# Kernel optimization log

Hardware: AMD Instinct MI355X
Metric: run time of the kernel (lower is better)

Reference implementation:

```python
import jax, jax.numpy as jnp
import numpy as np

T = 16                       # sample_duration
FG_THRESH, BG_HI, BG_LO = 0.5, 0.5, 0.1
ROIS_PER_IMAGE, FG_PER_IMAGE = 128, 32   # conf.TRAIN.BATCH_SIZE, round(0.25*128)
STDS = jnp.tile(jnp.array([0.1, 0.1, 0.2, 0.2], jnp.float32), T)  # BBOX_NORMALIZE_STDS tiled; means are 0


def _tube_iou(rois, gts):
    # rois [b,M,T,4], gts [b,K,T,4] -> mean per-frame IoU over non-empty frames [b,M,K]
    r = rois[:, :, None]             # [b,M,1,T,4]
    g = gts[:, None]                 # [b,1,K,T,4]
    iw = jnp.clip(jnp.minimum(r[..., 2], g[..., 2]) - jnp.maximum(r[..., 0], g[..., 0]) + 1.0, 0.0)
    ih = jnp.clip(jnp.minimum(r[..., 3], g[..., 3]) - jnp.maximum(r[..., 1], g[..., 1]) + 1.0, 0.0)
    inter = iw * ih
    ar = (r[..., 2] - r[..., 0] + 1.0) * (r[..., 3] - r[..., 1] + 1.0)
    ag = (g[..., 2] - g[..., 0] + 1.0) * (g[..., 3] - g[..., 1] + 1.0)
    r_empty = jnp.all(r == 0.0, -1)
    g_empty = jnp.all(g == 0.0, -1)
    iou = jnp.where(r_empty | g_empty, 0.0, inter / (ar + ag - inter))
    valid = ~(r_empty & g_empty)
    return iou.sum(-1) / jnp.maximum(valid.sum(-1), 1).astype(iou.dtype)


def _bbox_transform(ex, gt):
    ew = ex[..., 2] - ex[..., 0] + 1.0
    eh = ex[..., 3] - ex[..., 1] + 1.0
    ecx = ex[..., 0] + 0.5 * ew
    ecy = ex[..., 1] + 0.5 * eh
    gw = gt[..., 2] - gt[..., 0] + 1.0
    gh = gt[..., 3] - gt[..., 1] + 1.0
    gcx = gt[..., 0] + 0.5 * gw
    gcy = gt[..., 1] + 0.5 * gh
    return jnp.stack([(gcx - ecx) / ew, (gcy - ecy) / eh,
                      jnp.log(gw / ew), jnp.log(gh / eh)], axis=-1)


def _sample_one(ov, lab, key):
    # ov, lab: [M]; jit-safe fg/bg sampling matching the torch control flow
    M = ov.shape[0]
    k1, k2, k3, k4 = jax.random.split(key, 4)
    fg = ov >= FG_THRESH
    bg = (ov < BG_HI) & (ov >= BG_LO)
    fg_num = fg.sum()
    bg_num = bg.sum()
    # random permutation with fg (resp. bg) indices first
    order_fg = jnp.argsort(jnp.where(fg, jax.random.uniform(k1, (M,)), 2.0))
    order_bg = jnp.argsort(jnp.where(bg, jax.random.uniform(k2, (M,)), 2.0))
    fg_this = jnp.where(bg_num > 0, jnp.minimum(FG_PER_IMAGE, fg_num),
                        jnp.where(fg_num > 0, ROIS_PER_IMAGE, 0))
    r = jnp.arange(ROIS_PER_IMAGE)
    fg_repl = order_fg[(jax.random.uniform(k3, (ROIS_PER_IMAGE,)) * jnp.maximum(fg_num, 1)).astype(jnp.int32)]
    fg_idx = jnp.where(bg_num > 0, order_fg[r], fg_repl)  # no-replacement when bg exists, else with replacement
    bg_idx = order_bg[(jax.random.uniform(k4, (ROIS_PER_IMAGE,)) * jnp.maximum(bg_num, 1)).astype(jnp.int32)]
    is_fg = r < fg_this
    keep = jnp.where(is_fg, fg_idx, bg_idx)
    return keep, jnp.where(is_fg, lab[keep], 0.0)


def _forward(all_tubes, gt_boxes, gt_tubes_all):
    b, N, _ = all_tubes.shape
    A = gt_boxes.shape[1]
    # gt tube coords + label of first nonzero-labelled frame
    gt_tubes = gt_boxes[..., :4].reshape(b, A, T * 4)
    fr_lab = gt_boxes[..., 4]                                    # [b,A,T]
    has = jnp.any(fr_lab != 0, axis=2)
    first = jnp.argmax(fr_lab != 0, axis=2)
    labels_gt = jnp.where(has, jnp.take_along_axis(fr_lab, first[..., None], 2)[..., 0], 0.0)
    # scatter tube coords into frames [round(start), round(end)] (vectorized mask-scatter)
    sf = jnp.round(all_tubes[..., 3]).astype(jnp.int32)[..., None]
    ef = jnp.round(all_tubes[..., 6]).astype(jnp.int32)[..., None]
    f = jnp.arange(T)[None, None]
    fmask = ((f >= sf) & (f <= ef)).astype(all_tubes.dtype)      # [b,N,T]
    coords = all_tubes[..., jnp.array([1, 2, 4, 5])]             # [b,N,4]
    all_rois = fmask[..., None] * coords[:, :, None, :]          # [b,N,T,4]
    off = jnp.broadcast_to(jnp.arange(b, dtype=all_rois.dtype)[:, None, None], (b, N, 1))
    all_rois = jnp.concatenate([off, all_rois.reshape(b, N, T * 4)], axis=2)
    # append gt boxes/tubes as extra proposals (batch col = 0)
    gt_app = jnp.concatenate([jnp.zeros((b, A, 1), all_rois.dtype), gt_tubes], axis=2)
    all_rois = jnp.concatenate([all_rois, gt_app], axis=1)       # [b,N+A,1+4T]
    gt_tubes_app = jnp.concatenate([jnp.zeros((b, A, 1), all_tubes.dtype), gt_tubes_all[..., :-1]], axis=2)
    all_tubes_c = jnp.concatenate([all_tubes, gt_tubes_app], axis=1)  # [b,N+A,7]
    # IoU overlaps + gt assignment
    ov = _tube_iou(all_rois[..., 1:].reshape(b, N + A, T, 4),
                   gt_tubes.reshape(b, A, T, 4))                 # [b,N+A,A]
    max_ov = ov.max(axis=2)
    gt_asg = ov.argmax(axis=2)
    labels = jnp.take_along_axis(labels_gt, gt_asg, axis=1)      # [b,N+A]
    # fg/bg sampling (fixed key -> deterministic)
    keys = jax.random.split(jax.random.key(42), b)
    keep, labels_b = jax.vmap(_sample_one)(max_ov, labels, keys)  # [b,R]
    rois_b = jnp.take_along_axis(all_rois, keep[..., None], axis=1)
    rois_b = rois_b.at[..., 0].set(jnp.arange(b, dtype=rois_b.dtype)[:, None])
    tubes_b = jnp.take_along_axis(all_tubes_c, keep[..., None], axis=1)
    tubes_b = tubes_b.at[..., 0].set(jnp.arange(b, dtype=tubes_b.dtype)[:, None])
    asg_k = jnp.take_along_axis(gt_asg, keep, axis=1)
    gt_rois_b = jnp.take_along_axis(gt_tubes, asg_k[..., None], axis=1)  # [b,R,4T]
    tgt = _bbox_transform(rois_b[..., 1:].reshape(b, ROIS_PER_IMAGE, T, 4),
                          gt_rois_b.reshape(b, ROIS_PER_IMAGE, T, 4)).reshape(b, ROIS_PER_IMAGE, T * 4)
    tgt = tgt / STDS
    pos = (labels_b > 0)[..., None]
    bbox_targets = jnp.where(pos, tgt, 0.0)
    inside = jnp.where(pos, jnp.ones_like(tgt), 0.0)
    outside = (inside > 0).astype(tgt.dtype)
    return rois_b, tubes_b, labels_b, bbox_targets, inside, outside


def setup_inputs() -> dict:
    key = jax.random.key(0)
    ks = jax.random.split(key, 9)
    b, N, A = 8, 20000, 5
    x1 = jax.random.uniform(ks[0], (b, N), minval=0.0, maxval=200.0)
    y1 = jax.random.uniform(ks[1], (b, N), minval=0.0, maxval=200.0)
    x2 = x1 + jax.random.uniform(ks[2], (b, N), minval=8.0, maxval=120.0)
    y2 = y1 + jax.random.uniform(ks[3], (b, N), minval=8.0, maxval=120.0)
    sf = jax.random.randint(ks[4], (b, N), 0, T).astype(jnp.float32)
    ef = jnp.minimum(sf + jax.random.randint(ks[5], (b, N), 0, T).astype(jnp.float32), T - 1.0)
    bidx = jnp.broadcast_to(jnp.arange(b, dtype=jnp.float32)[:, None], (b, N))
    all_tubes = jnp.stack([bidx, x1, y1, sf, x2, y2, ef], axis=-1)
    gx1 = jax.random.uniform(ks[6], (b, A, T), minval=0.0, maxval=200.0)
    gy1 = jax.random.uniform(ks[7], (b, A, T), minval=0.0, maxval=200.0)
    gx2 = gx1 + 60.0
    gy2 = gy1 + 60.0
    glab = jax.random.randint(ks[8], (b, A), 1, 21).astype(jnp.float32)[..., None]
    gt_boxes = jnp.stack([gx1, gy1, gx2, gy2, jnp.broadcast_to(glab, (b, A, T))], axis=-1)
    gt_tubes_all = jnp.concatenate([
        jnp.zeros((b, A, 1)), gx1.min(-1, keepdims=True), gy1.min(-1, keepdims=True),
        jnp.zeros((b, A, 1)), gx2.max(-1, keepdims=True), gy2.max(-1, keepdims=True),
        jnp.full((b, A, 1), T - 1.0)], axis=-1).astype(jnp.float32)
    return {"all_tubes": all_tubes, "gt_boxes": gt_boxes, "gt_tubes_all": gt_tubes_all}


def reference(all_tubes, gt_boxes, gt_tubes_all):
    return _forward(all_tubes, gt_boxes, gt_tubes_all)
```

## Files before the change

### kernel.cpp

```cpp
#include <hip/hip_runtime.h>
#include <stdint.h>

#define T 16
#define NB 8
#define NROI 20000
#define NA 5
#define MM (NROI + NA)
#define MMPAD 20224
#define RPI 128
#define FGPI 32
#define NBLK 79
#define NBLK2 20
#define SORTCAP 32768
#define LCAP 16384
#define NBUCK 2048

__host__ __device__ __forceinline__ void tf2x32(uint32_t k0, uint32_t k1,
                                                uint32_t x0, uint32_t x1,
                                                uint32_t& o0, uint32_t& o1) {
  uint32_t ks2 = k0 ^ k1 ^ 0x1BD11BDAu;
  x0 += k0; x1 += k1;
#define ROUND(r) { x0 += x1; x1 = (x1 << (r)) | (x1 >> (32 - (r))); x1 ^= x0; }
  ROUND(13) ROUND(15) ROUND(26) ROUND(6)
  x0 += k1; x1 += ks2 + 1u;
  ROUND(17) ROUND(29) ROUND(16) ROUND(24)
  x0 += ks2; x1 += k0 + 2u;
  ROUND(13) ROUND(15) ROUND(26) ROUND(6)
  x0 += k0; x1 += k1 + 3u;
  ROUND(17) ROUND(29) ROUND(16) ROUND(24)
  x0 += k1; x1 += ks2 + 4u;
  ROUND(13) ROUND(15) ROUND(26) ROUND(6)
  x0 += ks2; x1 += k0 + 5u;
#undef ROUND
  o0 = x0; o1 = x1;
}

__device__ __forceinline__ uint32_t rbits32(uint32_t k0, uint32_t k1, uint32_t i) {
  uint32_t a, b; tf2x32(k0, k1, 0u, i, a, b); return a ^ b;
}
__device__ __forceinline__ float uni01(uint32_t bits) {
  return __uint_as_float((bits >> 9) | 0x3f800000u) - 1.0f;
}

struct Keys { uint32_t k[NB][4][2]; };

__global__ __launch_bounds__(256) void k_iou(const float* __restrict__ tubes,
                                             const float* __restrict__ gtb,
                                             float* __restrict__ ov) {
  int img = blockIdx.y;
  int a = blockIdx.z;
  int b = blockIdx.x;
  int tid = threadIdx.x;
  int n = b * 256 + tid;
  bool valid = n < MM;
  int nn = valid ? n : MM - 1;
  bool isroi = nn < NROI;

  __shared__ float tub[256 * 7];
  __shared__ float4 g4[NA][T];
  __shared__ float gar[NA][T];
  {
    int rcnt = min(256, NROI - b * 256);
    int f4cnt = (rcnt * 7) >> 2;
    const float4* src = (const float4*)(tubes + (size_t)img * NROI * 7 + (size_t)b * 256 * 7);
    float4* dst = (float4*)tub;
    for (int i = tid; i < f4cnt; i += 256) dst[i] = src[i];
  }
  for (int i = tid; i < NA * T; i += 256) {
    int aa = i / T, t = i - aa * T;
    const float* p = gtb + (((size_t)img * NA + aa) * T + t) * 5;
    float4 v = make_float4(p[0], p[1], p[2], p[3]);
    g4[aa][t] = v;
    gar[aa][t] = (v.z - v.x + 1.0f) * (v.w - v.y + 1.0f);
  }
  __syncthreads();

  float s = 0.0f;
  if (isroi) {
    const float* p = &tub[tid * 7];
    float rx1 = p[1], ry1 = p[2], rx2 = p[4], ry2 = p[5];
    int sf = (int)rintf(p[3]), ef = (int)rintf(p[6]);
    float rar = (rx2 - rx1 + 1.0f) * (ry2 - ry1 + 1.0f);
#pragma unroll
    for (int t = 0; t < T; ++t) {
      float4 gg = g4[a][t]; float ag = gar[a][t];
      float iw = fmaxf(fminf(rx2, gg.z) - fmaxf(rx1, gg.x) + 1.0f, 0.0f);
      float ih = fmaxf(fminf(ry2, gg.w) - fmaxf(ry1, gg.y) + 1.0f, 0.0f);
      float inter = iw * ih;
      float q = inter / (rar + ag - inter);
      s += ((t >= sf) && (t <= ef)) ? q : 0.0f;
    }
  } else {
    int ga = nn - NROI;
#pragma unroll
    for (int t = 0; t < T; ++t) {
      float4 e = g4[ga][t]; float ar = gar[ga][t];
      float4 gg = g4[a][t]; float ag = gar[a][t];
      float iw = fmaxf(fminf(e.z, gg.z) - fmaxf(e.x, gg.x) + 1.0f, 0.0f);
      float ih = fmaxf(fminf(e.w, gg.w) - fmaxf(e.y, gg.y) + 1.0f, 0.0f);
      float inter = iw * ih;
      s += inter / (ar + ag - inter);
    }
  }
  if (valid) ov[((size_t)img * NA + a) * MMPAD + n] = s / 16.0f;
}

__global__ __launch_bounds__(1024) void k_classify(const float* __restrict__ ov,
                                                   unsigned char* __restrict__ asg,
                                                   uint64_t* __restrict__ slots,
                                                   int* __restrict__ cnts2,
                                                   int* __restrict__ mins2,
                                                   Keys keys) {
  int img = blockIdx.y;
  int b = blockIdx.x;
  int tid = threadIdx.x;
  int n = b * 1024 + tid;
  bool valid = n < MM;
  int nn = valid ? n : MM - 1;
  int lane = tid & 63;
  int w = tid >> 6;

  const float* base_ov = ov + (size_t)img * NA * MMPAD + nn;
  float o0 = base_ov[0 * MMPAD];
  float o1 = base_ov[1 * MMPAD];
  float o2 = base_ov[2 * MMPAD];
  float o3 = base_ov[3 * MMPAD];
  float o4 = base_ov[4 * MMPAD];
  float best = o0; int barg = 0;
  if (o1 > best) { best = o1; barg = 1; }
  if (o2 > best) { best = o2; barg = 2; }
  if (o3 > best) { best = o3; barg = 3; }
  if (o4 > best) { best = o4; barg = 4; }

  if (valid) asg[(size_t)img * MM + n] = (unsigned char)barg;

  bool isfg = valid && (best >= 0.5f);
  bool isbg = valid && (best < 0.5f) && (best >= 0.1f);

  __shared__ int wcnt[16][2];
  __shared__ int wmn[16][2];
  unsigned long long mfg = __ballot(isfg);
  unsigned long long mbg = __ballot(isbg);
  unsigned long long mnf = __ballot(valid && !isfg);
  unsigned long long mnb = __ballot(valid && !isbg);
  int wavebase = b * 1024 + w * 64;
  if (lane == 0) {
    wcnt[w][0] = __popcll(mfg);
    wcnt[w][1] = __popcll(mbg);
    wmn[w][0] = mnf ? (wavebase + __ffsll(mnf) - 1) : 0x7FFFFFFF;
    wmn[w][1] = mnb ? (wavebase + __ffsll(mnb) - 1) : 0x7FFFFFFF;
  }
  __syncthreads();

  if (tid == 0) {
    int tf = 0, tb = 0, mf = 0x7FFFFFFF, mb = 0x7FFFFFFF;
#pragma unroll
    for (int w2 = 0; w2 < 16; ++w2) {
      tf += wcnt[w2][0]; tb += wcnt[w2][1];
      mf = min(mf, wmn[w2][0]); mb = min(mb, wmn[w2][1]);
    }
    int idx = img * NBLK2 + b;
    cnts2[idx]                = tf;
    cnts2[NB * NBLK2 + idx]   = tb;
    mins2[idx]                = mf;
    mins2[NB * NBLK2 + idx]   = mb;
  }

  int pf = 0, pb = 0;
  for (int w2 = 0; w2 < w; ++w2) { pf += wcnt[w2][0]; pb += wcnt[w2][1]; }
  unsigned long long below = (1ULL << lane) - 1ULL;
  uint64_t* slotF = slots + (size_t)(img * 2 + 0) * SORTCAP + b * 1024;
  uint64_t* slotB = slots + (size_t)(img * 2 + 1) * SORTCAP + b * 1024;
  if (isfg) {
    int pos = pf + __popcll(mfg & below);
    uint32_t m = rbits32(keys.k[img][0][0], keys.k[img][0][1], (uint32_t)n) >> 9;
    slotF[pos] = ((uint64_t)m << 32) | (uint32_t)n;
  }
  if (isbg) {
    int pos = pb + __popcll(mbg & below);
    uint32_t m = rbits32(keys.k[img][1][0], keys.k[img][1][1], (uint32_t)n) >> 9;
    slotB[pos] = ((uint64_t)m << 32) | (uint32_t)n;
  }
}

__global__ __launch_bounds__(1024) void k_sortsample(const float* __restrict__ tubes,
                                                     const float* __restrict__ gtb,
                                                     const float* __restrict__ gta,
                                                     const unsigned char* __restrict__ asg,
                                                     uint64_t* __restrict__ slots,
                                                     const int* __restrict__ cnts2,
                                                     const int* __restrict__ mins2,
                                                     Keys keys,
                                                     float* __restrict__ out) {
  __shared__ uint64_t buf[LCAP];
  __shared__ int hist[NBUCK];
  __shared__ int pref[NBUCK + 1];
  __shared__ int wsum[16];
  __shared__ int scnt[NBLK2], spref[NBLK2 + 1];
  __shared__ int s_tot, s_oth, s_mn;
  __shared__ int s_keep[RPI];
  __shared__ int s_ak[RPI];
  __shared__ float s_lab[RPI];
  __shared__ unsigned char s_own[RPI];

  int list = blockIdx.x;
  int img = list >> 1;
  int which = list & 1;
  int tid = threadIdx.x;
  int lane = tid & 63, wv = tid >> 6;
  uint64_t* arr = slots + (size_t)(img * 2 + which) * SORTCAP;
  const int* cn = cnts2 + which * NB * NBLK2 + img * NBLK2;
  const int* co = cnts2 + (1 - which) * NB * NBLK2 + img * NBLK2;
  const int* mn = mins2 + which * NB * NBLK2 + img * NBLK2;

  if (tid < NBLK2) scnt[tid] = cn[tid];
  for (int i = tid; i < NBUCK; i += 1024) hist[i] = 0;
  __syncthreads();
  if (tid == 0) {
    int acc = 0, mmn = 0x7FFFFFFF, oth = 0;
#pragma unroll
    for (int bb = 0; bb < NBLK2; ++bb) {
      spref[bb] = acc; acc += scnt[bb];
      mmn = min(mmn, mn[bb]); oth += co[bb];
    }
    spref[NBLK2] = acc; s_tot = acc; s_mn = mmn; s_oth = oth;
  }
  __syncthreads();
  int cnt = s_tot, min_non = s_mn;
  int fg_num = (which == 0) ? cnt : s_oth;
  int bg_num = (which == 0) ? s_oth : cnt;
  bool ldsPath = (cnt <= LCAP);

  if (cnt > 0 && ldsPath) {
    for (int s = tid; s < NBLK2 * 1024; s += 1024) {
      int bb = s >> 10, i = s & 1023;
      if (i < scnt[bb]) {
        uint64_t key = arr[s];
        atomicAdd(&hist[(int)(key >> 44)], 1);
      }
    }
    __syncthreads();
    {
      int a0 = hist[2 * tid], a1 = hist[2 * tid + 1];
      int ps = a0 + a1;
      int v = ps;
      for (int off = 1; off < 64; off <<= 1) {
        int u = __shfl_up(v, off);
        if (lane >= off) v += u;
      }
      if (lane == 63) wsum[wv] = v;
      __syncthreads();
      if (tid == 0) {
        int acc = 0;
        for (int i = 0; i < 16; ++i) { int x = wsum[i]; wsum[i] = acc; acc += x; }
        pref[NBUCK] = acc;
      }
      __syncthreads();
      int excl = v - ps + wsum[wv];
      pref[2 * tid] = excl;
      pref[2 * tid + 1] = excl + a0;
      hist[2 * tid] = excl;
      hist[2 * tid + 1] = excl + a0;
    }
    __syncthreads();
    for (int s = tid; s < NBLK2 * 1024; s += 1024) {
      int bb = s >> 10, i = s & 1023;
      if (i < scnt[bb]) {
        uint64_t key = arr[s];
        int pos = atomicAdd(&hist[(int)(key >> 44)], 1);
        buf[pos] = key;
      }
    }
    __syncthreads();
  } else if (cnt > 1) {
    for (int bb = 0; bb < NBLK2; ++bb) {
      uint64_t v = 0; int c = scnt[bb];
      if (tid < c) v = arr[bb * 1024 + tid];
      __syncthreads();
      if (tid < c) arr[spref[bb] + tid] = v;
      __syncthreads();
    }
    int n2 = 2; while (n2 < cnt) n2 <<= 1;
    for (int i = cnt + tid; i < n2; i += 1024) arr[i] = ~0ULL;
    __syncthreads();
    for (int k = 2; k <= n2; k <<= 1) {
      for (int j = k >> 1; j; j >>= 1) {
        for (int i = tid; i < n2; i += 1024) {
          int ixj = i ^ j;
          if (ixj > i) {
            uint64_t a = arr[i], bv = arr[ixj];
            bool up = (i & k) == 0;
            if (up ? (a > bv) : (a < bv)) { arr[i] = bv; arr[ixj] = a; }
          }
        }
        __syncthreads();
      }
    }
    __syncthreads();
  }

  float* o_rois = out;
  float* o_tub = out + (size_t)NB * RPI * 65;
  float* o_lab = o_tub + (size_t)NB * RPI * 7;
  float* o_tgt = o_lab + (size_t)NB * RPI;
  float* o_in  = o_tgt + (size_t)NB * RPI * 64;
  float* o_ou  = o_in  + (size_t)NB * RPI * 64;

  int fg_this = (bg_num > 0) ? min(FGPI, fg_num) : (fg_num > 0 ? RPI : 0);

#define RANKQ(L, OUTV) {                                               \
    int l_ = (L);                                                      \
    if (ldsPath) {                                                     \
      int lo_ = 0, hi_ = NBUCK;                                        \
      while (hi_ - lo_ > 1) {                                          \
        int mid_ = (lo_ + hi_) >> 1;                                   \
        if (pref[mid_] <= l_) lo_ = mid_; else hi_ = mid_;             \
      }                                                                \
      int base_ = pref[lo_], cnt_ = pref[lo_ + 1] - base_;             \
      int ll_ = l_ - base_;                                            \
      uint64_t ans_ = 0;                                               \
      for (int i_ = 0; i_ < cnt_; ++i_) {                              \
        uint64_t ki_ = buf[base_ + i_];                                \
        int cl_ = 0;                                                   \
        for (int j_ = 0; j_ < cnt_; ++j_) cl_ += (buf[base_ + j_] < ki_); \
        if (cl_ == ll_) { ans_ = ki_; break; }                         \
      }                                                                \
      OUTV = (int)(uint32_t)(ans_ & 0xffffffffULL);                    \
    } else {                                                           \
      OUTV = (int)(uint32_t)(arr[l_] & 0xffffffffULL);                 \
    }                                                                  \
  }

  if (tid < RPI) {
    int r = tid;
    bool is_fg = r < fg_this;
    bool own = (is_fg == (which == 0));
    s_own[r] = own ? 1 : 0;
    if (own) {
      int keep;
      if (which == 0) {
        if (bg_num > 0) {
          RANKQ(r, keep)
        } else {
          float u3 = uni01(rbits32(keys.k[img][2][0], keys.k[img][2][1], (uint32_t)r));
          int q = (int)(u3 * (float)max(fg_num, 1));
          if (q >= fg_num) {
            if (fg_num >= MM) { RANKQ(MM - 1, keep) } else keep = min_non;
          } else {
            RANKQ(q, keep)
          }
        }
      } else {
        float u4 = uni01(rbits32(keys.k[img][3][0], keys.k[img][3][1], (uint32_t)r));
        int qb = (int)(u4 * (float)max(bg_num, 1));
        if (qb >= bg_num) {
          if (bg_num >= MM) { RANKQ(MM - 1, keep) } else keep = min_non;
        } else {
          RANKQ(qb, keep)
        }
      }

      int ak = asg[(size_t)img * MM + keep];
      float glab = gtb[(((size_t)img * NA + ak) * T + 0) * 5 + 4];
      float lab = is_fg ? glab : 0.0f;
      s_keep[r] = keep; s_ak[r] = ak; s_lab[r] = lab;

      size_t row = (size_t)img * RPI + r;
      float* pt = o_tub + row * 7;
      o_rois[row * 65] = (float)img;
      pt[0] = (float)img;
      if (keep < NROI) {
        const float* p = tubes + ((size_t)img * NROI + keep) * 7;
#pragma unroll
        for (int cc = 1; cc < 7; ++cc) pt[cc] = p[cc];
      } else {
        const float* p = gta + ((size_t)img * NA + (keep - NROI)) * 7;
#pragma unroll
        for (int cc = 1; cc < 7; ++cc) pt[cc] = p[cc - 1];
      }
      o_lab[row] = lab;
    }
  }
#undef RANKQ
  __syncthreads();

  for (int i = tid; i < RPI * T; i += 1024) {
    int rl = i >> 4;
    if (!s_own[rl]) continue;
    int t = i & 15;
    size_t row = (size_t)img * RPI + rl;
    int keep = s_keep[rl];
    int ak = s_ak[rl];
    float lab = s_lab[rl];
    bool pos = lab > 0.0f;
    float posf = pos ? 1.0f : 0.0f;

    float ex1, ey1, ex2, ey2;
    if (keep < NROI) {
      const float* p = tubes + ((size_t)img * NROI + keep) * 7;
      int sf = (int)rintf(p[3]), ef = (int)rintf(p[6]);
      bool in = (t >= sf) && (t <= ef);
      ex1 = in ? p[1] : 0.0f; ey1 = in ? p[2] : 0.0f;
      ex2 = in ? p[4] : 0.0f; ey2 = in ? p[5] : 0.0f;
    } else {
      const float* p = gtb + (((size_t)img * NA + (keep - NROI)) * T + t) * 5;
      ex1 = p[0]; ey1 = p[1]; ex2 = p[2]; ey2 = p[3];
    }

    float* pr = o_rois + row * 65 + 1 + 4 * t;
    pr[0] = ex1; pr[1] = ey1; pr[2] = ex2; pr[3] = ey2;

    const float* gp = gtb + (((size_t)img * NA + ak) * T + t) * 5;
    float gx1 = gp[0], gy1 = gp[1], gx2 = gp[2], gy2 = gp[3];
    float ew = ex2 - ex1 + 1.0f, eh = ey2 - ey1 + 1.0f;
    float ecx = ex1 + 0.5f * ew, ecy = ey1 + 0.5f * eh;
    float gw = gx2 - gx1 + 1.0f, gh = gy2 - gy1 + 1.0f;
    float gcx = gx1 + 0.5f * gw, gcy = gy1 + 0.5f * gh;
    float t0 = ((gcx - ecx) / ew) / 0.1f;
    float t1 = ((gcy - ecy) / eh) / 0.1f;
    float t2 = logf(gw / ew) / 0.2f;
    float t3 = logf(gh / eh) / 0.2f;

    *(float4*)(o_tgt + row * 64 + 4 * t) =
        make_float4(pos ? t0 : 0.0f, pos ? t1 : 0.0f, pos ? t2 : 0.0f, pos ? t3 : 0.0f);
    float4 pf4 = make_float4(posf, posf, posf, posf);
    *(float4*)(o_in + row * 64 + 4 * t) = pf4;
    *(float4*)(o_ou + row * 64 + 4 * t) = pf4;
  }
}

extern "C" void kernel_launch(void* const* d_in, const int* in_sizes, int n_in,
                              void* d_out, int out_size, void* d_ws, size_t ws_size,
                              hipStream_t stream) {
  const float* tubes = (const float*)d_in[0];
  const float* gtb   = (const float*)d_in[1];
  const float* gta   = (const float*)d_in[2];
  float* out = (float*)d_out;
  char* ws = (char*)d_ws;

  Keys keys;
  for (int img = 0; img < NB; ++img) {
    uint32_t r0, r1; tf2x32(0u, 42u, 0u, (uint32_t)img, r0, r1);
    for (int j = 0; j < 4; ++j) {
      uint32_t a, b; tf2x32(r0, r1, 0u, (uint32_t)j, a, b);
      keys.k[img][j][0] = a; keys.k[img][j][1] = b;
    }
  }

  int* cnts2 = (int*)ws;
  int* mins2 = (int*)(ws + 1280);
  unsigned char* asg = (unsigned char*)(ws + 2560);
  uint64_t* slots = (uint64_t*)(ws + 162600);
  float* ov = (float*)(ws + 4356904);

  dim3 gI(NBLK, NB, NA);
  k_iou<<<gI, 256, 0, stream>>>(tubes, gtb, ov);
  dim3 gC(NBLK2, NB);
  k_classify<<<gC, 1024, 0, stream>>>(ov, asg, slots, cnts2, mins2, keys);
  k_sortsample<<<16, 1024, 0, stream>>>(tubes, gtb, gta, asg, slots, cnts2, mins2, keys, out);
}
```

Baseline: 39.20 us.

## Fuse classify and sort-sample kernels using a last-block-done atomic counter

```diff
diff --git a/kernel.cpp b/kernel.cpp
--- a/kernel.cpp
+++ b/kernel.cpp
@@ -46,11 +46,13 @@
 
 __global__ __launch_bounds__(256) void k_iou(const float* __restrict__ tubes,
                                              const float* __restrict__ gtb,
-                                             float* __restrict__ ov) {
+                                             float* __restrict__ ov,
+                                             int* __restrict__ donecnt) {
   int img = blockIdx.y;
   int a = blockIdx.z;
   int b = blockIdx.x;
   int tid = threadIdx.x;
+  if (img == 0 && a == 0 && b == 0 && tid < NB) donecnt[tid] = 0;
   int n = b * 256 + tid;
   bool valid = n < MM;
   int nn = valid ? n : MM - 1;
@@ -105,199 +107,121 @@
   if (valid) ov[((size_t)img * NA + a) * MMPAD + n] = s / 16.0f;
 }
 
-__global__ __launch_bounds__(1024) void k_classify(const float* __restrict__ ov,
-                                                   unsigned char* __restrict__ asg,
-                                                   uint64_t* __restrict__ slots,
-                                                   int* __restrict__ cnts2,
-                                                   int* __restrict__ mins2,
-                                                   Keys keys) {
-  int img = blockIdx.y;
-  int b = blockIdx.x;
-  int tid = threadIdx.x;
-  int n = b * 1024 + tid;
-  bool valid = n < MM;
-  int nn = valid ? n : MM - 1;
-  int lane = tid & 63;
-  int w = tid >> 6;
-
-  const float* base_ov = ov + (size_t)img * NA * MMPAD + nn;
-  float o0 = base_ov[0 * MMPAD];
-  float o1 = base_ov[1 * MMPAD];
-  float o2 = base_ov[2 * MMPAD];
-  float o3 = base_ov[3 * MMPAD];
-  float o4 = base_ov[4 * MMPAD];
-  float best = o0; int barg = 0;
-  if (o1 > best) { best = o1; barg = 1; }
-  if (o2 > best) { best = o2; barg = 2; }
-  if (o3 > best) { best = o3; barg = 3; }
-  if (o4 > best) { best = o4; barg = 4; }
-
-  if (valid) asg[(size_t)img * MM + n] = (unsigned char)barg;
-
-  bool isfg = valid && (best >= 0.5f);
-  bool isbg = valid && (best < 0.5f) && (best >= 0.1f);
-
-  __shared__ int wcnt[16][2];
-  __shared__ int wmn[16][2];
-  unsigned long long mfg = __ballot(isfg);
-  unsigned long long mbg = __ballot(isbg);
-  unsigned long long mnf = __ballot(valid && !isfg);
-  unsigned long long mnb = __ballot(valid && !isbg);
-  int wavebase = b * 1024 + w * 64;
-  if (lane == 0) {
-    wcnt[w][0] = __popcll(mfg);
-    wcnt[w][1] = __popcll(mbg);
-    wmn[w][0] = mnf ? (wavebase + __ffsll(mnf) - 1) : 0x7FFFFFFF;
-    wmn[w][1] = mnb ? (wavebase + __ffsll(mnb) - 1) : 0x7FFFFFFF;
-  }
-  __syncthreads();
-
-  if (tid == 0) {
-    int tf = 0, tb = 0, mf = 0x7FFFFFFF, mb = 0x7FFFFFFF;
-#pragma unroll
-    for (int w2 = 0; w2 < 16; ++w2) {
-      tf += wcnt[w2][0]; tb += wcnt[w2][1];
-      mf = min(mf, wmn[w2][0]); mb = min(mb, wmn[w2][1]);
-    }
-    int idx = img * NBLK2 + b;
-    cnts2[idx]                = tf;
-    cnts2[NB * NBLK2 + idx]   = tb;
-    mins2[idx]                = mf;
-    mins2[NB * NBLK2 + idx]   = mb;
-  }
-
-  int pf = 0, pb = 0;
-  for (int w2 = 0; w2 < w; ++w2) { pf += wcnt[w2][0]; pb += wcnt[w2][1]; }
-  unsigned long long below = (1ULL << lane) - 1ULL;
-  uint64_t* slotF = slots + (size_t)(img * 2 + 0) * SORTCAP + b * 1024;
-  uint64_t* slotB = slots + (size_t)(img * 2 + 1) * SORTCAP + b * 1024;
-  if (isfg) {
-    int pos = pf + __popcll(mfg & below);
-    uint32_t m = rbits32(keys.k[img][0][0], keys.k[img][0][1], (uint32_t)n) >> 9;
-    slotF[pos] = ((uint64_t)m << 32) | (uint32_t)n;
-  }
-  if (isbg) {
-    int pos = pb + __popcll(mbg & below);
-    uint32_t m = rbits32(keys.k[img][1][0], keys.k[img][1][1], (uint32_t)n) >> 9;
-    slotB[pos] = ((uint64_t)m << 32) | (uint32_t)n;
-  }
-}
-
-__global__ __launch_bounds__(1024) void k_sortsample(const float* __restrict__ tubes,
-                                                     const float* __restrict__ gtb,
-                                                     const float* __restrict__ gta,
-                                                     const unsigned char* __restrict__ asg,
-                                                     uint64_t* __restrict__ slots,
-                                                     const int* __restrict__ cnts2,
-                                                     const int* __restrict__ mins2,
-                                                     Keys keys,
-                                                     float* __restrict__ out) {
+__global__ __launch_bounds__(1024) void k_fused(const float* __restrict__ tubes,
+                                                const float* __restrict__ gtb,
+                                                const float* __restrict__ gta,
+                                                const float* __restrict__ ov,
+                                                unsigned char* __restrict__ asg,
+                                                uint64_t* __restrict__ slots,
+                                                int* __restrict__ cnts2,
+                                                int* __restrict__ mins2,
+                                                int* __restrict__ donecnt,
+                                                Keys keys,
+                                                float* __restrict__ out) {
   __shared__ uint64_t buf[LCAP];
   __shared__ int hist[NBUCK];
   __shared__ int pref[NBUCK + 1];
   __shared__ int wsum[16];
   __shared__ int scnt[NBLK2], spref[NBLK2 + 1];
-  __shared__ int s_tot, s_oth, s_mn;
+  __shared__ int wcnt[16][2], wmn[16][2];
+  __shared__ int s_last;
+  __shared__ int s_fgnum, s_bgnum, s_mnf, s_mnb, s_tot;
   __shared__ int s_keep[RPI];
   __shared__ int s_ak[RPI];
   __shared__ float s_lab[RPI];
-  __shared__ unsigned char s_own[RPI];
-
-  int list = blockIdx.x;
-  int img = list >> 1;
-  int which = list & 1;
+
+  int img = blockIdx.y;
+  int b = blockIdx.x;
   int tid = threadIdx.x;
-  int lane = tid & 63, wv = tid >> 6;
-  uint64_t* arr = slots + (size_t)(img * 2 + which) * SORTCAP;
-  const int* cn = cnts2 + which * NB * NBLK2 + img * NBLK2;
-  const int* co = cnts2 + (1 - which) * NB * NBLK2 + img * NBLK2;
-  const int* mn = mins2 + which * NB * NBLK2 + img * NBLK2;
-
-  if (tid < NBLK2) scnt[tid] = cn[tid];
-  for (int i = tid; i < NBUCK; i += 1024) hist[i] = 0;
+  int lane = tid & 63;
+  int w = tid >> 6;
+
+  {
+    int n = b * 1024 + tid;
+    bool valid = n < MM;
+    int nn = valid ? n : MM - 1;
+    const float* base_ov = ov + (size_t)img * NA * MMPAD + nn;
+    float o0 = base_ov[0 * MMPAD];
+    float o1 = base_ov[1 * MMPAD];
+    float o2 = base_ov[2 * MMPAD];
+    float o3 = base_ov[3 * MMPAD];
+    float o4 = base_ov[4 * MMPAD];
+    float best = o0; int barg = 0;
+    if (o1 > best) { best = o1; barg = 1; }
+    if (o2 > best) { best = o2; barg = 2; }
+    if (o3 > best) { best = o3; barg = 3; }
+    if (o4 > best) { best = o4; barg = 4; }
+
+    if (valid) asg[(size_t)img * MM + n] = (unsigned char)barg;
+
+    bool isfg = valid && (best >= 0.5f);
+    bool isbg = valid && (best < 0.5f) && (best >= 0.1f);
+
+    unsigned long long mfg = __ballot(isfg);
+    unsigned long long mbg = __ballot(isbg);
+    unsigned long long mnf = __ballot(valid && !isfg);
+    unsigned long long mnb = __ballot(valid && !isbg);
+    int wavebase = b * 1024 + w * 64;
+    if (lane == 0) {
+      wcnt[w][0] = __popcll(mfg);
+      wcnt[w][1] = __popcll(mbg);
+      wmn[w][0] = mnf ? (wavebase + __ffsll(mnf) - 1) : 0x7FFFFFFF;
+      wmn[w][1] = mnb ? (wavebase + __ffsll(mnb) - 1) : 0x7FFFFFFF;
+    }
+    __syncthreads();
+
+    if (tid == 0) {
+      int tf = 0, tb = 0, mf = 0x7FFFFFFF, mb = 0x7FFFFFFF;
+#pragma unroll
+      for (int w2 = 0; w2 < 16; ++w2) {
+        tf += wcnt[w2][0]; tb += wcnt[w2][1];
+        mf = min(mf, wmn[w2][0]); mb = min(mb, wmn[w2][1]);
+      }
+      int idx = img * NBLK2 + b;
+      cnts2[idx]                = tf;
+      cnts2[NB * NBLK2 + idx]   = tb;
+      mins2[idx]                = mf;
+      mins2[NB * NBLK2 + idx]   = mb;
+    }
+
+    int pf = 0, pb = 0;
+    for (int w2 = 0; w2 < w; ++w2) { pf += wcnt[w2][0]; pb += wcnt[w2][1]; }
+    unsigned long long below = (1ULL << lane) - 1ULL;
+    uint64_t* slotF = slots + (size_t)(img * 2 + 0) * SORTCAP + b * 1024;
+    uint64_t* slotB = slots + (size_t)(img * 2 + 1) * SORTCAP + b * 1024;
+    if (isfg) {
+      int pos = pf + __popcll(mfg & below);
+      uint32_t m = rbits32(keys.k[img][0][0], keys.k[img][0][1], (uint32_t)n) >> 9;
+      slotF[pos] = ((uint64_t)m << 32) | (uint32_t)n;
+    }
+    if (isbg) {
+      int pos = pb + __popcll(mbg & below);
+      uint32_t m = rbits32(keys.k[img][1][0], keys.k[img][1][1], (uint32_t)n) >> 9;
+      slotB[pos] = ((uint64_t)m << 32) | (uint32_t)n;
+    }
+  }
+
+  __threadfence();
+  if (tid == 0) s_last = (atomicAdd(&donecnt[img], 1) == NBLK2 - 1) ? 1 : 0;
   __syncthreads();
+  if (!s_last) return;
+  __threadfence();
+
   if (tid == 0) {
-    int acc = 0, mmn = 0x7FFFFFFF, oth = 0;
+    int tf = 0, tb = 0, mf = 0x7FFFFFFF, mb = 0x7FFFFFFF;
 #pragma unroll
     for (int bb = 0; bb < NBLK2; ++bb) {
-      spref[bb] = acc; acc += scnt[bb];
-      mmn = min(mmn, mn[bb]); oth += co[bb];
-    }
-    spref[NBLK2] = acc; s_tot = acc; s_mn = mmn; s_oth = oth;
+      tf += cnts2[img * NBLK2 + bb];
+      tb += cnts2[NB * NBLK2 + img * NBLK2 + bb];
+      mf = min(mf, mins2[img * NBLK2 + bb]);
+      mb = min(mb, mins2[NB * NBLK2 + img * NBLK2 + bb]);
+    }
+    s_fgnum = tf; s_bgnum = tb; s_mnf = mf; s_mnb = mb;
   }
   __syncthreads();
-  int cnt = s_tot, min_non = s_mn;
-  int fg_num = (which == 0) ? cnt : s_oth;
-  int bg_num = (which == 0) ? s_oth : cnt;
-  bool ldsPath = (cnt <= LCAP);
-
-  if (cnt > 0 && ldsPath) {
-    for (int s = tid; s < NBLK2 * 1024; s += 1024) {
-      int bb = s >> 10, i = s & 1023;
-      if (i < scnt[bb]) {
-        uint64_t key = arr[s];
-        atomicAdd(&hist[(int)(key >> 44)], 1);
-      }
-    }
-    __syncthreads();
-    {
-      int a0 = hist[2 * tid], a1 = hist[2 * tid + 1];
-      int ps = a0 + a1;
-      int v = ps;
-      for (int off = 1; off < 64; off <<= 1) {
-        int u = __shfl_up(v, off);
-        if (lane >= off) v += u;
-      }
-      if (lane == 63) wsum[wv] = v;
-      __syncthreads();
-      if (tid == 0) {
-        int acc = 0;
-        for (int i = 0; i < 16; ++i) { int x = wsum[i]; wsum[i] = acc; acc += x; }
-        pref[NBUCK] = acc;
-      }
-      __syncthreads();
-      int excl = v - ps + wsum[wv];
-      pref[2 * tid] = excl;
-      pref[2 * tid + 1] = excl + a0;
-      hist[2 * tid] = excl;
-      hist[2 * tid + 1] = excl + a0;
-    }
-    __syncthreads();
-    for (int s = tid; s < NBLK2 * 1024; s += 1024) {
-      int bb = s >> 10, i = s & 1023;
-      if (i < scnt[bb]) {
-        uint64_t key = arr[s];
-        int pos = atomicAdd(&hist[(int)(key >> 44)], 1);
-        buf[pos] = key;
-      }
-    }
-    __syncthreads();
-  } else if (cnt > 1) {
-    for (int bb = 0; bb < NBLK2; ++bb) {
-      uint64_t v = 0; int c = scnt[bb];
-      if (tid < c) v = arr[bb * 1024 + tid];
-      __syncthreads();
-      if (tid < c) arr[spref[bb] + tid] = v;
-      __syncthreads();
-    }
-    int n2 = 2; while (n2 < cnt) n2 <<= 1;
-    for (int i = cnt + tid; i < n2; i += 1024) arr[i] = ~0ULL;
-    __syncthreads();
-    for (int k = 2; k <= n2; k <<= 1) {
-      for (int j = k >> 1; j; j >>= 1) {
-        for (int i = tid; i < n2; i += 1024) {
-          int ixj = i ^ j;
-          if (ixj > i) {
-            uint64_t a = arr[i], bv = arr[ixj];
-            bool up = (i & k) == 0;
-            if (up ? (a > bv) : (a < bv)) { arr[i] = bv; arr[ixj] = a; }
-          }
-        }
-        __syncthreads();
-      }
-    }
-    __syncthreads();
-  }
+  int fg_num = s_fgnum, bg_num = s_bgnum;
+  int min_nonfg = s_mnf, min_nonbg = s_mnb;
+  int fg_this = (bg_num > 0) ? min(FGPI, fg_num) : (fg_num > 0 ? RPI : 0);
 
   float* o_rois = out;
   float* o_tub = out + (size_t)NB * RPI * 65;
@@ -306,7 +230,87 @@
   float* o_in  = o_tgt + (size_t)NB * RPI * 64;
   float* o_ou  = o_in  + (size_t)NB * RPI * 64;
 
-  int fg_this = (bg_num > 0) ? min(FGPI, fg_num) : (fg_num > 0 ? RPI : 0);
+  for (int which = 0; which < 2; ++which) {
+    uint64_t* arr = slots + (size_t)(img * 2 + which) * SORTCAP;
+    int cnt = (which == 0) ? fg_num : bg_num;
+    int min_non = (which == 0) ? min_nonfg : min_nonbg;
+    bool ldsPath = (cnt <= LCAP);
+
+    if (tid < NBLK2) scnt[tid] = cnts2[which * NB * NBLK2 + img * NBLK2 + tid];
+    for (int i = tid; i < NBUCK; i += 1024) hist[i] = 0;
+    __syncthreads();
+    if (tid == 0) {
+      int acc = 0;
+#pragma unroll
+      for (int bb = 0; bb < NBLK2; ++bb) { spref[bb] = acc; acc += scnt[bb]; }
+      spref[NBLK2] = acc; s_tot = acc;
+    }
+    __syncthreads();
+
+    if (cnt > 0 && ldsPath) {
+      for (int s = tid; s < NBLK2 * 1024; s += 1024) {
+        int bb = s >> 10, i = s & 1023;
+        if (i < scnt[bb]) atomicAdd(&hist[(int)(arr[s] >> 44)], 1);
+      }
+      __syncthreads();
+      {
+        int a0 = hist[2 * tid], a1 = hist[2 * tid + 1];
+        int ps = a0 + a1;
+        int v = ps;
+        for (int off = 1; off < 64; off <<= 1) {
+          int u = __shfl_up(v, off);
+          if (lane >= off) v += u;
+        }
+        if (lane == 63) wsum[w] = v;
+        __syncthreads();
+        if (tid == 0) {
+          int acc = 0;
+          for (int i = 0; i < 16; ++i) { int x = wsum[i]; wsum[i] = acc; acc += x; }
+          pref[NBUCK] = acc;
+        }
+        __syncthreads();
+        int excl = v - ps + wsum[w];
+        pref[2 * tid] = excl;
+        pref[2 * tid + 1] = excl + a0;
+        hist[2 * tid] = excl;
+        hist[2 * tid + 1] = excl + a0;
+      }
+      __syncthreads();
+      for (int s = tid; s < NBLK2 * 1024; s += 1024) {
+        int bb = s >> 10, i = s & 1023;
+        if (i < scnt[bb]) {
+          uint64_t key = arr[s];
+          int pos = atomicAdd(&hist[(int)(key >> 44)], 1);
+          buf[pos] = key;
+        }
+      }
+      __syncthreads();
+    } else if (cnt > 1) {
+      for (int bb = 0; bb < NBLK2; ++bb) {
+        uint64_t v = 0; int c = scnt[bb];
+        if (tid < c) v = arr[bb * 1024 + tid];
+        __syncthreads();
+        if (tid < c) arr[spref[bb] + tid] = v;
+        __syncthreads();
+      }
+      int n2 = 2; while (n2 < cnt) n2 <<= 1;
+      for (int i = cnt + tid; i < n2; i += 1024) arr[i] = ~0ULL;
+      __syncthreads();
+      for (int k = 2; k <= n2; k <<= 1) {
+        for (int j = k >> 1; j; j >>= 1) {
+          for (int i = tid; i < n2; i += 1024) {
+            int ixj = i ^ j;
+            if (ixj > i) {
+              uint64_t a = arr[i], bv = arr[ixj];
+              bool up = (i & k) == 0;
+              if (up ? (a > bv) : (a < bv)) { arr[i] = bv; arr[ixj] = a; }
+            }
+          }
+          __syncthreads();
+        }
+      }
+      __syncthreads();
+    }
 
 #define RANKQ(L, OUTV) {                                               \
     int l_ = (L);                                                      \
@@ -331,62 +335,61 @@
     }                                                                  \
   }
 
-  if (tid < RPI) {
-    int r = tid;
-    bool is_fg = r < fg_this;
-    bool own = (is_fg == (which == 0));
-    s_own[r] = own ? 1 : 0;
-    if (own) {
-      int keep;
-      if (which == 0) {
-        if (bg_num > 0) {
-          RANKQ(r, keep)
+    if (tid < RPI) {
+      int r = tid;
+      bool is_fg = r < fg_this;
+      bool own = (is_fg == (which == 0));
+      if (own) {
+        int keep;
+        if (which == 0) {
+          if (bg_num > 0) {
+            RANKQ(r, keep)
+          } else {
+            float u3 = uni01(rbits32(keys.k[img][2][0], keys.k[img][2][1], (uint32_t)r));
+            int q = (int)(u3 * (float)max(fg_num, 1));
+            if (q >= fg_num) {
+              if (fg_num >= MM) { RANKQ(MM - 1, keep) } else keep = min_non;
+            } else {
+              RANKQ(q, keep)
+            }
+          }
         } else {
-          float u3 = uni01(rbits32(keys.k[img][2][0], keys.k[img][2][1], (uint32_t)r));
-          int q = (int)(u3 * (float)max(fg_num, 1));
-          if (q >= fg_num) {
-            if (fg_num >= MM) { RANKQ(MM - 1, keep) } else keep = min_non;
+          float u4 = uni01(rbits32(keys.k[img][3][0], keys.k[img][3][1], (uint32_t)r));
+          int qb = (int)(u4 * (float)max(bg_num, 1));
+          if (qb >= bg_num) {
+            if (bg_num >= MM) { RANKQ(MM - 1, keep) } else keep = min_non;
           } else {
-            RANKQ(q, keep)
+            RANKQ(qb, keep)
           }
         }
-      } else {
-        float u4 = uni01(rbits32(keys.k[img][3][0], keys.k[img][3][1], (uint32_t)r));
-        int qb = (int)(u4 * (float)max(bg_num, 1));
-        if (qb >= bg_num) {
-          if (bg_num >= MM) { RANKQ(MM - 1, keep) } else keep = min_non;
+
+        int ak = asg[(size_t)img * MM + keep];
+        float glab = gtb[(((size_t)img * NA + ak) * T + 0) * 5 + 4];
+        float lab = is_fg ? glab : 0.0f;
+        s_keep[r] = keep; s_ak[r] = ak; s_lab[r] = lab;
+
+        size_t row = (size_t)img * RPI + r;
+        float* pt = o_tub + row * 7;
+        o_rois[row * 65] = (float)img;
+        pt[0] = (float)img;
+        if (keep < NROI) {
+          const float* p = tubes + ((size_t)img * NROI + keep) * 7;
+#pragma unroll
+          for (int cc = 1; cc < 7; ++cc) pt[cc] = p[cc];
         } else {
-          RANKQ(qb, keep)
-        }
-      }
-
-      int ak = asg[(size_t)img * MM + keep];
-      float glab = gtb[(((size_t)img * NA + ak) * T + 0) * 5 + 4];
-      float lab = is_fg ? glab : 0.0f;
-      s_keep[r] = keep; s_ak[r] = ak; s_lab[r] = lab;
-
-      size_t row = (size_t)img * RPI + r;
-      float* pt = o_tub + row * 7;
-      o_rois[row * 65] = (float)img;
-      pt[0] = (float)img;
-      if (keep < NROI) {
-        const float* p = tubes + ((size_t)img * NROI + keep) * 7;
-#pragma unroll
-        for (int cc = 1; cc < 7; ++cc) pt[cc] = p[cc];
-      } else {
-        const float* p = gta + ((size_t)img * NA + (keep - NROI)) * 7;
-#pragma unroll
-        for (int cc = 1; cc < 7; ++cc) pt[cc] = p[cc - 1];
-      }
-      o_lab[row] = lab;
-    }
-  }
+          const float* p = gta + ((size_t)img * NA + (keep - NROI)) * 7;
+#pragma unroll
+          for (int cc = 1; cc < 7; ++cc) pt[cc] = p[cc - 1];
+        }
+        o_lab[row] = lab;
+      }
+    }
 #undef RANKQ
-  __syncthreads();
+    __syncthreads();
+  }
 
   for (int i = tid; i < RPI * T; i += 1024) {
     int rl = i >> 4;
-    if (!s_own[rl]) continue;
     int t = i & 15;
     size_t row = (size_t)img * RPI + rl;
     int keep = s_keep[rl];
@@ -449,13 +452,13 @@
 
   int* cnts2 = (int*)ws;
   int* mins2 = (int*)(ws + 1280);
-  unsigned char* asg = (unsigned char*)(ws + 2560);
-  uint64_t* slots = (uint64_t*)(ws + 162600);
-  float* ov = (float*)(ws + 4356904);
+  int* donecnt = (int*)(ws + 2560);
+  unsigned char* asg = (unsigned char*)(ws + 2688);
+  uint64_t* slots = (uint64_t*)(ws + 162728);
+  float* ov = (float*)(ws + 4357032);
 
   dim3 gI(NBLK, NB, NA);
-  k_iou<<<gI, 256, 0, stream>>>(tubes, gtb, ov);
+  k_iou<<<gI, 256, 0, stream>>>(tubes, gtb, ov, donecnt);
   dim3 gC(NBLK2, NB);
-  k_classify<<<gC, 1024, 0, stream>>>(ov, asg, slots, cnts2, mins2, keys);
-  k_sortsample<<<16, 1024, 0, stream>>>(tubes, gtb, gta, asg, slots, cnts2, mins2, keys, out);
-}
+  k_fused<<<gC, 1024, 0, stream>>>(tubes, gtb, gta, ov, asg, slots, cnts2, mins2, donecnt, keys, out);
+}
```

New measurement: 89.08 us. +127.3%, slower.
